# Kernel optimization log

Hardware: AMD Instinct MI355X
Metric: run time of the kernel (lower is better)

The kernel has to match this reference:

```python
import jax, jax.numpy as jnp
import numpy as np

K_NN = 20
EPS = 1e-5

def _conv1(x, w):
    # 1x1 Conv1d: w [O,C], x [B,C,N] -> [B,O,N]
    return jnp.einsum('oc,bcn->bon', w, x)

def _bn_eval(x, g, b):
    # BatchNorm1d in eval mode with running_mean=0, running_var=1
    return x * (g / np.sqrt(1.0 + EPS))[None, :, None] + b[None, :, None]

def _gn(x, g, b, groups=32):
    B, C, N = x.shape
    xr = x.reshape(B, groups, C // groups, N)
    mu = xr.mean(axis=(2, 3), keepdims=True)
    var = xr.var(axis=(2, 3), keepdims=True)
    xn = ((xr - mu) * jax.lax.rsqrt(var + EPS)).reshape(B, C, N)
    return xn * g[None, :, None] + b[None, :, None]

def _lrelu(x):
    return jnp.where(x >= 0, x, 0.2 * x)

def _graph_cross_attention(x, y, k):
    # x:[B,C,N] query features, y:[B,C,M] key features
    xn = x / jnp.linalg.norm(x, axis=1, keepdims=True)
    yn = y / jnp.linalg.norm(y, axis=1, keepdims=True)
    simi = jnp.einsum('bcn,bcm->bnm', xn, yn)          # cosine similarity [B,N,M]
    s, idx = jax.lax.top_k(simi, k)                    # [B,N,k] values and indices
    yt = jnp.swapaxes(y, 1, 2)                         # [B,M,C]
    nn = jax.vmap(lambda yb, ib: yb[ib])(yt, idx)      # gather neighbors [B,N,k,C]
    xt = jnp.swapaxes(x, 1, 2)                         # [B,N,C]
    diff = nn - xt[:, :, None, :]                      # edge features
    w = jax.nn.softmax(s, axis=-1)                     # attention over k neighbors
    agg = jnp.einsum('bnk,bnkc->bnc', w, diff)         # weighted aggregation
    return jnp.swapaxes(jnp.concatenate([xt, agg], axis=-1), 1, 2)  # [B,2C,N]

def setup_inputs() -> dict:
    key = jax.random.key(0)
    ks = jax.random.split(key, 22)
    B, N = 8, 2048
    f = lambda k, s: jax.random.normal(k, s, dtype=jnp.float32)
    return {
        'x1': f(ks[0], (B, 64, N)),
        'x2': f(ks[1], (B, 64, N)),
        'x3': f(ks[2], (B, 128, N)),
        'y3': f(ks[3], (B, 128, N)),
        'w4': f(ks[4], (256, 256)) * 0.06,
        'bn4_g': 1.0 + 0.1 * f(ks[5], (256,)),
        'bn4_b': 0.1 * f(ks[6], (256,)),
        'w5': f(ks[7], (512, 512)) * 0.04,
        'gn5_g': 1.0 + 0.1 * f(ks[8], (512,)),
        'gn5_b': 0.1 * f(ks[9], (512,)),
        'wm1': f(ks[10], (512, 512)) * 0.04,
        'bm1': 0.02 * f(ks[11], (512,)),
        'gn6_g': 1.0 + 0.1 * f(ks[12], (512,)),
        'gn6_b': 0.1 * f(ks[13], (512,)),
        'wm2': f(ks[14], (256, 512)) * 0.04,
        'bm2': 0.02 * f(ks[15], (256,)),
        'gn7_g': 1.0 + 0.1 * f(ks[16], (256,)),
        'gn7_b': 0.1 * f(ks[17], (256,)),
        'wm3': f(ks[18], (128, 256)) * 0.06,
        'bm3': 0.02 * f(ks[19], (128,)),
        'gn8_g': 1.0 + 0.1 * f(ks[20], (128,)),
        'gn8_b': 0.1 * f(ks[21], (128,)),
    }

def reference(x1, x2, x3, y3, w4, bn4_g, bn4_b, w5, gn5_g, gn5_b, wm1, bm1, gn6_g, gn6_b, wm2, bm2, gn7_g, gn7_b, wm3, bm3, gn8_g, gn8_b):
    x = _graph_cross_attention(x3, y3, K_NN)                  # [B,256,N]
    x4 = _lrelu(_bn_eval(_conv1(x, w4), bn4_g, bn4_b))        # conv4 [B,256,N]
    x = jnp.concatenate([x1, x2, x3, x4], axis=1)             # [B,512,N]
    local_concat = _lrelu(_gn(_conv1(x, w5), gn5_g, gn5_b))   # conv5 [B,512,N]
    gmax = local_concat.max(axis=2)
    gavg = local_concat.mean(axis=2)
    global_vector = jnp.concatenate([gmax, gavg], axis=1)     # [B,1024]
    h = jax.nn.relu(_gn(_conv1(local_concat, wm1) + bm1[None, :, None], gn6_g, gn6_b))
    h = jax.nn.relu(_gn(_conv1(h, wm2) + bm2[None, :, None], gn7_g, gn7_b))
    emb = jax.nn.relu(_gn(_conv1(h, wm3) + bm3[None, :, None], gn8_g, gn8_b))
    return emb, global_vector[:, :, None]
```

## Files before the change

kernel.cpp:

```cpp
#include <hip/hip_runtime.h>
#include <math.h>

#define N2 2048
#define LRELU_S 0.2f
#define BN4_RS 0.9999950000374997f

typedef short bf16x8 __attribute__((ext_vector_type(8)));
typedef float f32x16 __attribute__((ext_vector_type(16)));

__device__ __forceinline__ unsigned short bhi(float v) { return (unsigned short)(__float_as_uint(v) >> 16); }
__device__ __forceinline__ float bhif(float v) { return __uint_as_float(__float_as_uint(v) & 0xFFFF0000u); }
__device__ __forceinline__ float bf2f(unsigned short u) { return __uint_as_float(((unsigned int)u) << 16); }

__device__ __forceinline__ void gl16(const void* g, void* l) {
    __builtin_amdgcn_global_load_lds((const __attribute__((address_space(1))) unsigned int*)g,
                                     (__attribute__((address_space(3))) unsigned int*)l, 16, 0, 0);
}

__device__ __forceinline__ f32x16 z16() {
    f32x16 v;
    #pragma unroll
    for (int i = 0; i < 16; ++i) v[i] = 0.f;
    return v;
}

#define MFMA32 __builtin_amdgcn_mfma_f32_32x32x16_bf16

template<int ASRC, int EPI, int PASSES>
__global__ __launch_bounds__(256) void mgemm(
    const unsigned short* __restrict__ a1H, const unsigned short* __restrict__ a1L, int CA,
    const unsigned short* __restrict__ a2H, const unsigned short* __restrict__ a2L,
    const unsigned short* __restrict__ a3H, const unsigned short* __restrict__ a3L,
    const unsigned short* __restrict__ a4H, const unsigned short* __restrict__ a4L,
    const unsigned short* __restrict__ bH,  const unsigned short* __restrict__ bL, long bBs,
    int Ktot, int OC, int bbase,
    float* __restrict__ outF, unsigned short* __restrict__ oH,
    const float* __restrict__ epg, const float* __restrict__ epb,
    float* __restrict__ cs1, float* __restrict__ cs2)
{
    __shared__ alignas(16) unsigned short lAh[4096], lBh[4096];
    __shared__ alignas(16) unsigned short lAl[PASSES == 3 ? 4096 : 16];
    __shared__ alignas(16) unsigned short lBl[PASSES == 3 ? 4096 : 16];
    const int t  = threadIdx.x;
    const int n0 = blockIdx.x * 128;
    const int o0 = blockIdx.y * 128;
    const int bz = blockIdx.z;
    const int b  = bbase + bz;

    const int lane = t & 63;
    const int h    = lane >> 5;
    const int l31  = lane & 31;
    const int wid  = t >> 6;
    const int wm   = wid >> 1;
    const int wn   = wid & 1;
    const int sw   = (l31 >> 1) & 3;

    f32x16 acc00 = z16(), acc01 = z16(), acc10 = z16(), acc11 = z16();

    const int q0 = t, q1 = t + 256;
    const int r0 = q0 >> 2, p0 = q0 & 3, c0s = p0 ^ ((r0 >> 1) & 3);
    const int r1 = q1 >> 2, p1 = q1 & 3, c1s = p1 ^ ((r1 >> 1) & 3);

    const int rA0 = (wm * 64 + l31) * 32, rA1 = rA0 + 1024;
    const int rB0 = (wn * 64 + l31) * 32, rB1 = rB0 + 1024;

    for (int kc = 0; kc < Ktot; kc += 32) {
        const unsigned short *sAH, *sAL; int koff, Cs;
        if (ASRC == 0)      { sAH = a1H; sAL = a1L; koff = kc;       Cs = CA; }
        else if (ASRC == 1) {
            if (kc < 128)   { sAH = a1H; sAL = a1L; koff = kc;       Cs = 128; }
            else            { sAH = a2H; sAL = a2L; koff = kc - 128; Cs = 128; }
        } else {
            if (kc < 64)        { sAH = a1H; sAL = a1L; koff = kc;       Cs = 64;  }
            else if (kc < 128)  { sAH = a2H; sAL = a2L; koff = kc - 64;  Cs = 64;  }
            else if (kc < 256)  { sAH = a3H; sAL = a3L; koff = kc - 128; Cs = 128; }
            else                { sAH = a4H; sAL = a4L; koff = kc - 256; Cs = 256; }
        }
        __syncthreads();
        {
            long ga = ((long)b * N2 + n0 + r0) * Cs + koff + c0s * 8;
            long gb = (long)b * bBs + (long)(o0 + r0) * Ktot + kc + c0s * 8;
            gl16(sAH + ga, lAh + q0 * 8);
            gl16(bH + gb, lBh + q0 * 8);
            if (PASSES == 3) { gl16(sAL + ga, lAl + q0 * 8); gl16(bL + gb, lBl + q0 * 8); }
            long ga1 = ((long)b * N2 + n0 + r1) * Cs + koff + c1s * 8;
            long gb1 = (long)b * bBs + (long)(o0 + r1) * Ktot + kc + c1s * 8;
            gl16(sAH + ga1, lAh + q1 * 8);
            gl16(bH + gb1, lBh + q1 * 8);
            if (PASSES == 3) { gl16(sAL + ga1, lAl + q1 * 8); gl16(bL + gb1, lBl + q1 * 8); }
        }
        __syncthreads();
        #pragma unroll
        for (int s = 0; s < 2; ++s) {
            const int off = ((s * 2 + h) ^ sw) * 8;
            bf16x8 a0h = *(const bf16x8*)(lAh + rA0 + off);
            bf16x8 a1h_ = *(const bf16x8*)(lAh + rA1 + off);
            bf16x8 b0h = *(const bf16x8*)(lBh + rB0 + off);
            bf16x8 b1h = *(const bf16x8*)(lBh + rB1 + off);
            acc00 = MFMA32(a0h, b0h, acc00, 0, 0, 0);
            acc01 = MFMA32(a0h, b1h, acc01, 0, 0, 0);
            acc10 = MFMA32(a1h_, b0h, acc10, 0, 0, 0);
            acc11 = MFMA32(a1h_, b1h, acc11, 0, 0, 0);
            if (PASSES == 3) {
                bf16x8 a0l = *(const bf16x8*)(lAl + rA0 + off);
                bf16x8 a1l_ = *(const bf16x8*)(lAl + rA1 + off);
                bf16x8 b0l = *(const bf16x8*)(lBl + rB0 + off);
                bf16x8 b1l = *(const bf16x8*)(lBl + rB1 + off);
                acc00 = MFMA32(a0h, b0l, acc00, 0, 0, 0);
                acc00 = MFMA32(a0l, b0h, acc00, 0, 0, 0);
                acc01 = MFMA32(a0h, b1l, acc01, 0, 0, 0);
                acc01 = MFMA32(a0l, b1h, acc01, 0, 0, 0);
                acc10 = MFMA32(a1h_, b0l, acc10, 0, 0, 0);
                acc10 = MFMA32(a1l_, b0h, acc10, 0, 0, 0);
                acc11 = MFMA32(a1h_, b1l, acc11, 0, 0, 0);
                acc11 = MFMA32(a1l_, b1h, acc11, 0, 0, 0);
            }
        }
    }

    #pragma unroll
    for (int ni = 0; ni < 2; ++ni) {
        const int o = o0 + wn * 64 + ni * 32 + l31;
        float sc = 0.f, sh = 0.f, bias = 0.f;
        if (EPI == 1) { sc = epg[o] * BN4_RS; sh = epb[o]; }
        if (EPI == 2) { bias = epb ? epb[o] : 0.f; }
        float s1 = 0.f, s2 = 0.f;
        #pragma unroll
        for (int mi = 0; mi < 2; ++mi) {
            #pragma unroll
            for (int r = 0; r < 16; ++r) {
                const int n = n0 + wm * 64 + mi * 32 + (r & 3) + 8 * (r >> 2) + 4 * h;
                float v = (ni == 0) ? (mi == 0 ? acc00[r] : acc10[r])
                                    : (mi == 0 ? acc01[r] : acc11[r]);
                const long oi = ((long)bz * N2 + n) * (long)OC + o;
                if (EPI == 0) {
                    outF[oi] = v;
                } else if (EPI == 1) {
                    v = fmaf(v, sc, sh);
                    v = v >= 0.f ? v : LRELU_S * v;
                    oH[oi] = bhi(v);
                } else {
                    v += bias;
                    outF[oi] = v;
                    s1 += v; s2 = fmaf(v, v, s2);
                }
            }
        }
        if (EPI == 2) {
            s1 += __shfl_xor(s1, 32);
            s2 += __shfl_xor(s2, 32);
            if (h == 0) {
                atomicAdd(cs1 + bz * OC + o, s1);
                atomicAdd(cs2 + bz * OC + o, s2);
            }
        }
    }
}

__global__ void normK(const float* __restrict__ x3, const float* __restrict__ y3,
                      float* __restrict__ invnx, float* __restrict__ invny)
{
    const int n = blockIdx.x * 256 + threadIdx.x;
    const int b = blockIdx.y;
    const float* src = blockIdx.z ? y3 : x3;
    float ss = 0.f;
    for (int c = 0; c < 128; ++c) {
        float v = src[((long)b * 128 + c) * N2 + n];
        ss = fmaf(v, v, ss);
    }
    (blockIdx.z ? invny : invnx)[b * N2 + n] = rsqrtf(ss);
}

template<int MODE>
__global__ __launch_bounds__(256) void tsplitK(
    const float* __restrict__ in, int C,
    unsigned short* __restrict__ tHi, const float* __restrict__ invn,
    unsigned short* __restrict__ sHi, unsigned short* __restrict__ sLo,
    float* __restrict__ tF)
{
    __shared__ float lt[64 * 65];
    const int t = threadIdx.x;
    const int n0 = blockIdx.x * 64, c0 = blockIdx.y * 64, b = blockIdx.z;
    {
        const int nl = t & 63;
        const int cb = t >> 6;
        #pragma unroll
        for (int i = 0; i < 16; ++i) {
            const int cl = cb + 4 * i;
            lt[nl * 65 + cl] = in[((long)b * C + c0 + cl) * N2 + n0 + nl];
        }
    }
    __syncthreads();
    const int cl = t & 63;
    const int nb = t >> 6;
    #pragma unroll
    for (int i = 0; i < 16; ++i) {
        const int nl = nb + 4 * i;
        const float v = lt[nl * 65 + cl];
        const long oi = ((long)b * N2 + n0 + nl) * C + c0 + cl;
        if (MODE & 1) tHi[oi] = bhi(v);
        if (MODE & 2) {
            const float svv = v * invn[b * N2 + n0 + nl];
            sHi[oi] = bhi(svv); sLo[oi] = bhi(svv - bhif(svv));
        }
        if (MODE & 4) tF[oi] = v;
    }
}

__global__ void wsplitK(const float* __restrict__ w4, const float* __restrict__ w5,
    const float* __restrict__ wm1, const float* __restrict__ wm2, const float* __restrict__ wm3,
    unsigned short* __restrict__ w4h, unsigned short* __restrict__ w5h,
    unsigned short* __restrict__ m1h, unsigned short* __restrict__ m2h,
    unsigned short* __restrict__ m3h)
{
    const int y = blockIdx.y;
    const int idx = blockIdx.x * 256 + threadIdx.x;
    float v; unsigned short* dh;
    if (y == 0) {
        if (idx >= 256 * 256) return;
        const int k = idx & 255;
        v = w4[idx];
        if (k < 128) v -= w4[idx + 128];
        dh = w4h;
    } else if (y == 1) {
        if (idx >= 512 * 512) return;
        v = w5[idx]; dh = w5h;
    } else if (y == 2) {
        if (idx >= 512 * 512) return;
        v = wm1[idx]; dh = m1h;
    } else if (y == 3) {
        if (idx >= 256 * 512) return;
        v = wm2[idx]; dh = m2h;
    } else {
        if (idx >= 128 * 256) return;
        v = wm3[idx]; dh = m3h;
    }
    dh[idx] = bhi(v);
}

__global__ __launch_bounds__(256) void topkK(const float* __restrict__ simi,
    float* __restrict__ topw, int* __restrict__ topi, int bbase)
{
    __shared__ unsigned int hist[256];
    __shared__ unsigned int bcast[2];
    __shared__ float lmn[4], lmx[4];
    __shared__ unsigned int cnt0, candCnt, tick;
    __shared__ unsigned int candU[256];
    __shared__ float candV[256];
    __shared__ int   candI[256];
    __shared__ float selv[20];
    __shared__ int   seli[20];
    const int t  = threadIdx.x;
    const int n  = blockIdx.x;
    const int bl = blockIdx.y;
    const float* row = simi + ((long)bl * N2 + n) * N2;

    float    f[8];
    unsigned u[8];
    {
        const float4 v0 = *(const float4*)(row + 4 * t);
        const float4 v1 = *(const float4*)(row + 1024 + 4 * t);
        f[0] = v0.x; f[1] = v0.y; f[2] = v0.z; f[3] = v0.w;
        f[4] = v1.x; f[5] = v1.y; f[6] = v1.z; f[7] = v1.w;
        #pragma unroll
        for (int i = 0; i < 8; ++i) {
            unsigned ub = __float_as_uint(f[i]);
            u[i] = ub ^ (((int)ub >> 31) | 0x80000000u);
        }
    }

    float tmn = f[0], tmx = f[0];
    #pragma unroll
    for (int i = 1; i < 8; ++i) { tmn = fminf(tmn, f[i]); tmx = fmaxf(tmx, f[i]); }
    #pragma unroll
    for (int off = 1; off < 64; off <<= 1) {
        tmn = fminf(tmn, __shfl_xor(tmn, off));
        tmx = fmaxf(tmx, __shfl_xor(tmx, off));
    }
    if ((t & 63) == 0) { lmn[t >> 6] = tmn; lmx[t >> 6] = tmx; }
    if (t == 0) { cnt0 = 0; candCnt = 0; tick = 0; }
    hist[t] = 0;
    __syncthreads();
    const float rmn = fminf(fminf(lmn[0], lmn[1]), fminf(lmn[2], lmn[3]));
    const float rmx = fmaxf(fmaxf(lmx[0], lmx[1]), fmaxf(lmx[2], lmx[3]));
    const float rng = rmx - rmn;
    const float scale = (rng > 0.f) ? (255.0f / rng) : 0.f;

    int q[8];
    #pragma unroll
    for (int i = 0; i < 8; ++i) {
        int qi = (int)((f[i] - rmn) * scale);
        q[i] = qi < 0 ? 0 : (qi > 255 ? 255 : qi);
        atomicAdd(&hist[q[i]], 1u);
    }
    __syncthreads();

    if (t < 64) {
        const unsigned h0 = hist[4 * t], h1 = hist[4 * t + 1];
        const unsigned h2 = hist[4 * t + 2], h3 = hist[4 * t + 3];
        const unsigned s3 = h3, s2 = h2 + s3, s1 = h1 + s2, s0 = h0 + s1;
        unsigned inc = s0;
        #pragma unroll
        for (int off = 1; off < 64; off <<= 1) {
            const unsigned o = __shfl_down(inc, off);
            if (t + off < 64) inc += o;
        }
        const unsigned excl = inc - s0;
        const unsigned sf[5] = {excl + s0, excl + s1, excl + s2, excl + s3, excl};
        #pragma unroll
        for (int j = 0; j < 4; ++j) {
            if (sf[j] >= 20u && sf[j + 1] < 20u) {
                bcast[0] = 4 * t + j;
                bcast[1] = 20u - sf[j + 1];
            }
        }
    }
    __syncthreads();
    const int Abin   = (int)bcast[0];
    const int kneedA = (int)bcast[1];
    const int gt     = 20 - kneedA;

    #pragma unroll
    for (int i = 0; i < 8; ++i) {
        const int idx = (i < 4) ? (4 * t + i) : (1024 + 4 * t + (i - 4));
        if (q[i] > Abin) {
            const unsigned s = atomicAdd(&cnt0, 1u);
            selv[s] = f[i]; seli[s] = idx;
        } else if (q[i] == Abin) {
            const unsigned s = atomicAdd(&candCnt, 1u);
            if (s < 256u) { candU[s] = u[i]; candV[s] = f[i]; candI[s] = idx; }
        }
    }
    __syncthreads();

    const int cc = (int)candCnt;
    if (cc <= 256) {
        for (int slot = t; slot < cc; slot += 256) {
            const unsigned ui = candU[slot];
            int r = 0;
            for (int j = 0; j < cc; ++j) {
                const unsigned uj = candU[j];
                r += (uj > ui) || (uj == ui && j < slot);
            }
            if (r < kneedA) { selv[gt + r] = candV[slot]; seli[gt + r] = candI[slot]; }
        }
    } else {
        #pragma unroll
        for (int i = 0; i < 8; ++i) {
            const int idx = (i < 4) ? (4 * t + i) : (1024 + 4 * t + (i - 4));
            if (q[i] == Abin) {
                const unsigned e = atomicAdd(&tick, 1u);
                if ((int)e < kneedA) { selv[gt + e] = f[i]; seli[gt + e] = idx; }
            }
        }
    }
    __syncthreads();

    if (t < 64) {
        const float v = (t < 20) ? selv[t] : -1e30f;
        float m = v;
        #pragma unroll
        for (int off = 1; off < 32; off <<= 1) m = fmaxf(m, __shfl_xor(m, off, 32));
        const float e = (t < 20) ? expf(v - m) : 0.f;
        float s = e;
        #pragma unroll
        for (int off = 1; off < 32; off <<= 1) s += __shfl_xor(s, off, 32);
        if (t < 20) {
            const long base = (((long)(bbase + bl)) * N2 + n) * 20;
            topw[base + t] = e / s;
            topi[base + t] = seli[t];
        }
    }
}

__global__ __launch_bounds__(256) void aggK(const float* __restrict__ yT,
    const float* __restrict__ topw, const int* __restrict__ topi,
    unsigned short* __restrict__ Gh)
{
    const int t  = threadIdx.x;
    const int c4 = (t & 31) * 4;
    const int ns = t >> 5;
    const int b  = blockIdx.x;
    const int n  = blockIdx.y * 8 + ns;
    const long tb = ((long)b * N2 + n) * 20;
    const float* yb = yT + (long)b * N2 * 128 + c4;

    float a0 = 0.f, a1 = 0.f, a2 = 0.f, a3 = 0.f;
    #pragma unroll
    for (int k = 0; k < 20; ++k) {
        const float w  = topw[tb + k];
        const int  idx = topi[tb + k];
        const float4 v = *(const float4*)(yb + (long)idx * 128);
        a0 = fmaf(w, v.x, a0);
        a1 = fmaf(w, v.y, a1);
        a2 = fmaf(w, v.z, a2);
        a3 = fmaf(w, v.w, a3);
    }
    const long oi = ((long)b * N2 + n) * 128 + c4;
    ushort4 hh;
    hh.x = bhi(a0); hh.y = bhi(a1); hh.z = bhi(a2); hh.w = bhi(a3);
    *(ushort4*)(Gh + oi) = hh;
}

__global__ void statsK(const float* __restrict__ cs1, const float* __restrict__ cs2,
    float* __restrict__ stats, int C)
{
    const int t = threadIdx.x;
    const int b = t >> 5, g = t & 31;
    const int cpg = C >> 5;
    float s1 = 0.f, s2 = 0.f;
    for (int j = 0; j < cpg; ++j) {
        s1 += cs1[b * C + g * cpg + j];
        s2 += cs2[b * C + g * cpg + j];
    }
    const float cnt = (float)(cpg * N2);
    const float mu = s1 / cnt;
    const float var = s2 / cnt - mu * mu;
    stats[t * 2] = mu;
    stats[t * 2 + 1] = rsqrtf(var + 1e-5f);
}

template<int ACT, int LC>
__global__ void gnapplyK(const float* __restrict__ pre, const float* __restrict__ stats,
    const float* __restrict__ gamma, const float* __restrict__ beta,
    unsigned short* __restrict__ oH)
{
    const long i4 = ((long)blockIdx.x * 256 + threadIdx.x) * 4;
    const int C = 1 << LC;
    const int c = (int)(i4 & (C - 1));
    const int bn = (int)(i4 >> LC);
    const int b = bn >> 11;
    const int g = c >> (LC - 5);
    const float mu = stats[(b * 32 + g) * 2];
    const float rs = stats[(b * 32 + g) * 2 + 1];
    const float4 gm = *(const float4*)(gamma + c);
    const float4 bt = *(const float4*)(beta + c);
    const float4 v = *(const float4*)(pre + i4);
    const float vals[4] = {v.x, v.y, v.z, v.w};
    const float gms[4] = {gm.x, gm.y, gm.z, gm.w};
    const float bts[4] = {bt.x, bt.y, bt.z, bt.w};
    unsigned short hs[4];
    #pragma unroll
    for (int j = 0; j < 4; ++j) {
        float x = (vals[j] - mu) * (rs * gms[j]) + bts[j];
        x = (ACT == 0) ? (x >= 0.f ? x : LRELU_S * x) : (x >= 0.f ? x : 0.f);
        hs[j] = bhi(x);
    }
    ushort4 hh; hh.x = hs[0]; hh.y = hs[1]; hh.z = hs[2]; hh.w = hs[3];
    *(ushort4*)(oH + i4) = hh;
}

__global__ __launch_bounds__(256) void gnfinalK(const float* __restrict__ pre,
    const float* __restrict__ stats, const float* __restrict__ gamma,
    const float* __restrict__ beta, float* __restrict__ out)
{
    __shared__ float lt[64 * 65];
    const int t = threadIdx.x;
    const int n0 = blockIdx.x * 64, c0 = blockIdx.y * 64, b = blockIdx.z;
    {
        const int cl = t & 63;
        const int nb = t >> 6;
        const int c = c0 + cl;
        const int g = c >> 2;
        const float mu = stats[(b * 32 + g) * 2];
        const float rs = stats[(b * 32 + g) * 2 + 1];
        const float sc = rs * gamma[c], sh = beta[c] - mu * sc;
        #pragma unroll
        for (int i = 0; i < 16; ++i) {
            const int nl = nb + 4 * i;
            float v = pre[((long)b * N2 + n0 + nl) * 128 + c];
            v = v * sc + sh;
            lt[cl * 65 + nl] = v > 0.f ? v : 0.f;
        }
    }
    __syncthreads();
    const int nl = t & 63;
    const int cb = t >> 6;
    #pragma unroll
    for (int i = 0; i < 16; ++i) {
        const int cl = cb + 4 * i;
        out[((long)b * 128 + c0 + cl) * N2 + n0 + nl] = lt[cl * 65 + nl];
    }
}

__global__ __launch_bounds__(256) void pool1K(const unsigned short* __restrict__ lcH,
    float* __restrict__ pmax, float* __restrict__ psum)
{
    __shared__ float lmx[512], lsm[512];
    const int t  = threadIdx.x;
    const int cq = t & 127;
    const int rp = t >> 7;
    const int nch = blockIdx.x;
    const int b   = blockIdx.y;
    float mx[4] = {-1e30f, -1e30f, -1e30f, -1e30f};
    float sm[4] = {0.f, 0.f, 0.f, 0.f};
    for (int i = 0; i < 32; ++i) {
        const int n = nch * 64 + 2 * i + rp;
        const long base = ((long)b * N2 + n) * 512 + cq * 4;
        const ushort4 hh = *(const ushort4*)(lcH + base);
        const float v0 = bf2f(hh.x);
        const float v1 = bf2f(hh.y);
        const float v2 = bf2f(hh.z);
        const float v3 = bf2f(hh.w);
        mx[0] = fmaxf(mx[0], v0); sm[0] += v0;
        mx[1] = fmaxf(mx[1], v1); sm[1] += v1;
        mx[2] = fmaxf(mx[2], v2); sm[2] += v2;
        mx[3] = fmaxf(mx[3], v3); sm[3] += v3;
    }
    if (rp) {
        #pragma unroll
        for (int j = 0; j < 4; ++j) { lmx[cq * 4 + j] = mx[j]; lsm[cq * 4 + j] = sm[j]; }
    }
    __syncthreads();
    if (!rp) {
        const long pb = ((long)(b * 32 + nch)) * 512 + cq * 4;
        #pragma unroll
        for (int j = 0; j < 4; ++j) {
            pmax[pb + j] = fmaxf(mx[j], lmx[cq * 4 + j]);
            psum[pb + j] = sm[j] + lsm[cq * 4 + j];
        }
    }
}

__global__ void pool2K(const float* __restrict__ pmax, const float* __restrict__ psum,
                       float* __restrict__ gv)
{
    const int t = threadIdx.x;
    const int b = blockIdx.x;
    float mx0 = -1e30f, mx1 = -1e30f, s0 = 0.f, s1 = 0.f;
    for (int nch = 0; nch < 32; ++nch) {
        const long pb = ((long)(b * 32 + nch)) * 512 + 2 * t;
        const float2 pm = *(const float2*)(pmax + pb);
        const float2 ps = *(const float2*)(psum + pb);
        mx0 = fmaxf(mx0, pm.x); mx1 = fmaxf(mx1, pm.y);
        s0 += ps.x; s1 += ps.y;
    }
    gv[b * 1024 + 2 * t]           = mx0;
    gv[b * 1024 + 2 * t + 1]       = mx1;
    gv[b * 1024 + 512 + 2 * t]     = s0 * (1.f / 2048.f);
    gv[b * 1024 + 512 + 2 * t + 1] = s1 * (1.f / 2048.f);
}

extern "C" void kernel_launch(void* const* d_in, const int* in_sizes, int n_in,
                              void* d_out, int out_size, void* d_ws, size_t ws_size,
                              hipStream_t stream)
{
    const float* x1    = (const float*)d_in[0];
    const float* x2    = (const float*)d_in[1];
    const float* x3    = (const float*)d_in[2];
    const float* y3    = (const float*)d_in[3];
    const float* w4    = (const float*)d_in[4];
    const float* bn4g  = (const float*)d_in[5];
    const float* bn4b  = (const float*)d_in[6];
    const float* w5    = (const float*)d_in[7];
    const float* gn5g  = (const float*)d_in[8];
    const float* gn5b  = (const float*)d_in[9];
    const float* wm1   = (const float*)d_in[10];
    const float* bm1   = (const float*)d_in[11];
    const float* gn6g  = (const float*)d_in[12];
    const float* gn6b  = (const float*)d_in[13];
    const float* wm2   = (const float*)d_in[14];
    const float* bm2   = (const float*)d_in[15];
    const float* gn7g  = (const float*)d_in[16];
    const float* gn7b  = (const float*)d_in[17];
    const float* wm3   = (const float*)d_in[18];
    const float* bm3   = (const float*)d_in[19];
    const float* gn8g  = (const float*)d_in[20];
    const float* gn8b  = (const float*)d_in[21];
    float* out = (float*)d_out;
    (void)in_sizes; (void)n_in; (void)out_size; (void)ws_size;

    char* ws = (char*)d_ws;
    float*          simiF = (float*)(ws + 0);
    float*          bufPS = (float*)(ws + 0);
    unsigned short* lcH   = (unsigned short*)(ws + 134217728);
    unsigned short* h1H   = (unsigned short*)(ws + 150994944);
    unsigned short* x4H   = (unsigned short*)(ws + 167772160);
    unsigned short* h2H   = (unsigned short*)(ws + 176160768);
    float*          yT    = (float*)(ws + 184549376);
    unsigned short* x3tH  = (unsigned short*)(ws + 192937984);
    unsigned short* GH    = (unsigned short*)(ws + 197132288);
    unsigned short* xnH   = (unsigned short*)(ws + 201326592);
    unsigned short* xnL   = (unsigned short*)(ws + 205520896);
    unsigned short* ynH   = (unsigned short*)(ws + 209715200);
    unsigned short* ynL   = (unsigned short*)(ws + 213909504);
    unsigned short* x1tH  = (unsigned short*)(ws + 218103808);
    unsigned short* x2tH  = (unsigned short*)(ws + 220200960);
    unsigned short* w4pH  = (unsigned short*)(ws + 222298112);
    unsigned short* w5H   = (unsigned short*)(ws + 222429184);
    unsigned short* m1H   = (unsigned short*)(ws + 222953472);
    unsigned short* m2H   = (unsigned short*)(ws + 223477760);
    unsigned short* m3H   = (unsigned short*)(ws + 223739904);
    float* invnx = (float*)(ws + 223805440);
    float* invny = (float*)(ws + 223870976);
    float* topw  = (float*)(ws + 223936512);
    int*   topi  = (int*)  (ws + 225247232);
    float* csb   = (float*)(ws + 226557952);
    float* cs1_5 = csb,          *cs2_5 = csb + 4096;
    float* cs1_6 = csb + 8192,   *cs2_6 = csb + 12288;
    float* cs1_7 = csb + 16384,  *cs2_7 = csb + 20480;
    float* cs1_8 = csb + 24576,  *cs2_8 = csb + 28672;
    float* stats5 = (float*)(ws + 226689024);
    float* stats6 = stats5 + 512;
    float* stats7 = stats5 + 1024;
    float* stats8 = stats5 + 1536;
    float* pmax  = (float*)(ws + 226697216);
    float* psum  = (float*)(ws + 227221504);

    const dim3 B256(256);
    const unsigned short* nu = nullptr;

    hipMemsetAsync(csb, 0, 131072, stream);

    normK<<<dim3(8, 8, 2), B256, 0, stream>>>(x3, y3, invnx, invny);
    tsplitK<6><<<dim3(32, 2, 8), B256, 0, stream>>>(y3, 128, nullptr, invny, ynH, ynL, yT);
    tsplitK<3><<<dim3(32, 2, 8), B256, 0, stream>>>(x3, 128, x3tH, invnx, xnH, xnL, nullptr);
    tsplitK<1><<<dim3(32, 1, 8), B256, 0, stream>>>(x1, 64, x1tH, nullptr, nullptr, nullptr, nullptr);
    tsplitK<1><<<dim3(32, 1, 8), B256, 0, stream>>>(x2, 64, x2tH, nullptr, nullptr, nullptr, nullptr);
    wsplitK<<<dim3(1024, 5), B256, 0, stream>>>(w4, w5, wm1, wm2, wm3,
        w4pH, w5H, m1H, m2H, m3H);

    mgemm<0, 0, 3><<<dim3(16, 16, 8), B256, 0, stream>>>(
        xnH, xnL, 128, nu, nu, nu, nu, nu, nu,
        ynH, ynL, (long)N2 * 128, 128, 2048, 0,
        simiF, nullptr, nullptr, nullptr, nullptr, nullptr);
    topkK<<<dim3(2048, 8), B256, 0, stream>>>(simiF, topw, topi, 0);

    aggK<<<dim3(8, 256), B256, 0, stream>>>(yT, topw, topi, GH);

    mgemm<1, 1, 1><<<dim3(16, 2, 8), B256, 0, stream>>>(
        x3tH, nu, 128, GH, nu, nu, nu, nu, nu,
        w4pH, nu, 0, 256, 256, 0,
        nullptr, x4H, bn4g, bn4b, nullptr, nullptr);

    mgemm<2, 2, 1><<<dim3(16, 4, 8), B256, 0, stream>>>(
        x1tH, nu, 64, x2tH, nu, x3tH, nu, x4H, nu,
        w5H, nu, 0, 512, 512, 0,
        bufPS, nullptr, nullptr, nullptr, cs1_5, cs2_5);
    statsK<<<1, B256, 0, stream>>>(cs1_5, cs2_5, stats5, 512);
    gnapplyK<0, 9><<<8192, B256, 0, stream>>>(bufPS, stats5, gn5g, gn5b, lcH);

    pool1K<<<dim3(32, 8), B256, 0, stream>>>(lcH, pmax, psum);
    pool2K<<<dim3(8), B256, 0, stream>>>(pmax, psum, out + (long)8 * 128 * 2048);

    mgemm<0, 2, 1><<<dim3(16, 4, 8), B256, 0, stream>>>(
        lcH, nu, 512, nu, nu, nu, nu, nu, nu,
        m1H, nu, 0, 512, 512, 0,
        bufPS, nullptr, nullptr, bm1, cs1_6, cs2_6);
    statsK<<<1, B256, 0, stream>>>(cs1_6, cs2_6, stats6, 512);
    gnapplyK<1, 9><<<8192, B256, 0, stream>>>(bufPS, stats6, gn6g, gn6b, h1H);

    mgemm<0, 2, 1><<<dim3(16, 2, 8), B256, 0, stream>>>(
        h1H, nu, 512, nu, nu, nu, nu, nu, nu,
        m2H, nu, 0, 512, 256, 0,
        bufPS, nullptr, nullptr, bm2, cs1_7, cs2_7);
    statsK<<<1, B256, 0, stream>>>(cs1_7, cs2_7, stats7, 256);
    gnapplyK<1, 8><<<4096, B256, 0, stream>>>(bufPS, stats7, gn7g, gn7b, h2H);

    mgemm<0, 2, 1><<<dim3(16, 1, 8), B256, 0, stream>>>(
        h2H, nu, 256, nu, nu, nu, nu, nu, nu,
        m3H, nu, 0, 256, 128, 0,
        bufPS, nullptr, nullptr, bm3, cs1_8, cs2_8);
    statsK<<<1, B256, 0, stream>>>(cs1_8, cs2_8, stats8, 128);
    gnfinalK<<<dim3(32, 2, 8), B256, 0, stream>>>(bufPS, stats8, gn8g, gn8b, out);
}
```

Measured before the change: 358.2 us.

## Fuse norm into transpose, fold GN stats into apply, add nontemporal simi traffic

The separate row-norm kernel is merged into a single transpose kernel that stages all 128 channels in LDS, computes the inverse norm there, and writes the normalized hi/lo bf16 splits. The two 64-channel transposes are merged into one launch. The four single-block statsK launches are removed; each GroupNorm apply block now recomputes its group mean and rstd from the channel sums. Nontemporal store and load hints are added on the similarity matrix write and its read in top-k. Together this cuts about six kernel launches and one pass over x3/y3, at the cost of redundant per-block stats work and a larger LDS tile in the transpose.

Measured after the change: 325.8 us. 1.1x faster.

```diff
diff --git a/kernel.cpp b/kernel.cpp
--- a/kernel.cpp
+++ b/kernel.cpp
@@ -7,6 +7,7 @@
 
 typedef short bf16x8 __attribute__((ext_vector_type(8)));
 typedef float f32x16 __attribute__((ext_vector_type(16)));
+typedef float f32x4 __attribute__((ext_vector_type(4)));
 
 __device__ __forceinline__ unsigned short bhi(float v) { return (unsigned short)(__float_as_uint(v) >> 16); }
 __device__ __forceinline__ float bhif(float v) { return __uint_as_float(__float_as_uint(v) & 0xFFFF0000u); }
@@ -134,7 +135,7 @@
                                     : (mi == 0 ? acc01[r] : acc11[r]);
                 const long oi = ((long)bz * N2 + n) * (long)OC + o;
                 if (EPI == 0) {
-                    outF[oi] = v;
+                    __builtin_nontemporal_store(v, outF + oi);
                 } else if (EPI == 1) {
                     v = fmaf(v, sc, sh);
                     v = v >= 0.f ? v : LRELU_S * v;
@@ -157,37 +158,67 @@
     }
 }
 
-__global__ void normK(const float* __restrict__ x3, const float* __restrict__ y3,
-                      float* __restrict__ invnx, float* __restrict__ invny)
-{
-    const int n = blockIdx.x * 256 + threadIdx.x;
-    const int b = blockIdx.y;
-    const float* src = blockIdx.z ? y3 : x3;
-    float ss = 0.f;
-    for (int c = 0; c < 128; ++c) {
-        float v = src[((long)b * 128 + c) * N2 + n];
-        ss = fmaf(v, v, ss);
-    }
-    (blockIdx.z ? invny : invnx)[b * N2 + n] = rsqrtf(ss);
-}
-
 template<int MODE>
-__global__ __launch_bounds__(256) void tsplitK(
-    const float* __restrict__ in, int C,
-    unsigned short* __restrict__ tHi, const float* __restrict__ invn,
-    unsigned short* __restrict__ sHi, unsigned short* __restrict__ sLo,
-    float* __restrict__ tF)
-{
-    __shared__ float lt[64 * 65];
+__global__ __launch_bounds__(256) void tnormK(
+    const float* __restrict__ in,
+    unsigned short* __restrict__ tHi, float* __restrict__ tF,
+    unsigned short* __restrict__ sHi, unsigned short* __restrict__ sLo)
+{
+    __shared__ float lt[64 * 130];
+    __shared__ float pinv[64];
     const int t = threadIdx.x;
-    const int n0 = blockIdx.x * 64, c0 = blockIdx.y * 64, b = blockIdx.z;
+    const int n0 = blockIdx.x * 64, b = blockIdx.z;
     {
         const int nl = t & 63;
         const int cb = t >> 6;
         #pragma unroll
+        for (int i = 0; i < 32; ++i) {
+            const int cl = cb + 4 * i;
+            lt[nl * 130 + cl] = in[((long)b * 128 + cl) * N2 + n0 + nl];
+        }
+    }
+    __syncthreads();
+    if (t < 64) {
+        float ss = 0.f;
+        for (int c = 0; c < 128; ++c) {
+            const float v = lt[t * 130 + c];
+            ss = fmaf(v, v, ss);
+        }
+        pinv[t] = rsqrtf(ss);
+    }
+    __syncthreads();
+    const int cl = t & 127;
+    const int nb = t >> 7;
+    #pragma unroll
+    for (int i = 0; i < 32; ++i) {
+        const int nl = nb + 2 * i;
+        const float v = lt[nl * 130 + cl];
+        const float sv = v * pinv[nl];
+        const long oi = ((long)b * N2 + n0 + nl) * 128 + cl;
+        sHi[oi] = bhi(sv); sLo[oi] = bhi(sv - bhif(sv));
+        if (MODE & 1) tHi[oi] = bhi(v);
+        if (MODE & 4) tF[oi] = v;
+    }
+}
+
+__global__ __launch_bounds__(256) void t64K(
+    const float* __restrict__ x1, const float* __restrict__ x2,
+    unsigned short* __restrict__ o1, unsigned short* __restrict__ o2)
+{
+    __shared__ float lt[64 * 65];
+    const int t = threadIdx.x;
+    const int z = blockIdx.z;
+    const int b = z & 7;
+    const float* in = (z < 8) ? x1 : x2;
+    unsigned short* outp = (z < 8) ? o1 : o2;
+    const int n0 = blockIdx.x * 64;
+    {
+        const int nl = t & 63;
+        const int cb = t >> 6;
+        #pragma unroll
         for (int i = 0; i < 16; ++i) {
             const int cl = cb + 4 * i;
-            lt[nl * 65 + cl] = in[((long)b * C + c0 + cl) * N2 + n0 + nl];
+            lt[nl * 65 + cl] = in[((long)b * 64 + cl) * N2 + n0 + nl];
         }
     }
     __syncthreads();
@@ -196,14 +227,7 @@
     #pragma unroll
     for (int i = 0; i < 16; ++i) {
         const int nl = nb + 4 * i;
-        const float v = lt[nl * 65 + cl];
-        const long oi = ((long)b * N2 + n0 + nl) * C + c0 + cl;
-        if (MODE & 1) tHi[oi] = bhi(v);
-        if (MODE & 2) {
-            const float svv = v * invn[b * N2 + n0 + nl];
-            sHi[oi] = bhi(svv); sLo[oi] = bhi(svv - bhif(svv));
-        }
-        if (MODE & 4) tF[oi] = v;
+        outp[((long)b * N2 + n0 + nl) * 64 + cl] = bhi(lt[nl * 65 + cl]);
     }
 }
 
@@ -258,10 +282,10 @@
     float    f[8];
     unsigned u[8];
     {
-        const float4 v0 = *(const float4*)(row + 4 * t);
-        const float4 v1 = *(const float4*)(row + 1024 + 4 * t);
-        f[0] = v0.x; f[1] = v0.y; f[2] = v0.z; f[3] = v0.w;
-        f[4] = v1.x; f[5] = v1.y; f[6] = v1.z; f[7] = v1.w;
+        const f32x4 v0 = __builtin_nontemporal_load((const f32x4*)(row + 4 * t));
+        const f32x4 v1 = __builtin_nontemporal_load((const f32x4*)(row + 1024 + 4 * t));
+        f[0] = v0[0]; f[1] = v0[1]; f[2] = v0[2]; f[3] = v0[3];
+        f[4] = v1[0]; f[5] = v1[1]; f[6] = v1[2]; f[7] = v1[3];
         #pragma unroll
         for (int i = 0; i < 8; ++i) {
             unsigned ub = __float_as_uint(f[i]);
@@ -402,37 +426,35 @@
     *(ushort4*)(Gh + oi) = hh;
 }
 
-__global__ void statsK(const float* __restrict__ cs1, const float* __restrict__ cs2,
-    float* __restrict__ stats, int C)
-{
-    const int t = threadIdx.x;
-    const int b = t >> 5, g = t & 31;
-    const int cpg = C >> 5;
-    float s1 = 0.f, s2 = 0.f;
-    for (int j = 0; j < cpg; ++j) {
-        s1 += cs1[b * C + g * cpg + j];
-        s2 += cs2[b * C + g * cpg + j];
-    }
-    const float cnt = (float)(cpg * N2);
-    const float mu = s1 / cnt;
-    const float var = s2 / cnt - mu * mu;
-    stats[t * 2] = mu;
-    stats[t * 2 + 1] = rsqrtf(var + 1e-5f);
-}
-
 template<int ACT, int LC>
-__global__ void gnapplyK(const float* __restrict__ pre, const float* __restrict__ stats,
+__global__ void gnapplyK(const float* __restrict__ pre,
+    const float* __restrict__ cs1, const float* __restrict__ cs2,
     const float* __restrict__ gamma, const float* __restrict__ beta,
     unsigned short* __restrict__ oH)
 {
-    const long i4 = ((long)blockIdx.x * 256 + threadIdx.x) * 4;
+    __shared__ float smu[32], srs[32];
     const int C = 1 << LC;
+    const int cpg = C >> 5;
+    const long blockBase = (long)blockIdx.x * 1024;
+    const int b = (int)(blockBase >> (LC + 11));
+    const int t = threadIdx.x;
+    if (t < 32) {
+        float s1 = 0.f, s2 = 0.f;
+        for (int j = 0; j < cpg; ++j) {
+            s1 += cs1[b * C + t * cpg + j];
+            s2 += cs2[b * C + t * cpg + j];
+        }
+        const float cnt = (float)(cpg * N2);
+        const float mu = s1 / cnt;
+        const float var = s2 / cnt - mu * mu;
+        smu[t] = mu; srs[t] = rsqrtf(var + 1e-5f);
+    }
+    __syncthreads();
+    const long i4 = blockBase + t * 4;
     const int c = (int)(i4 & (C - 1));
-    const int bn = (int)(i4 >> LC);
-    const int b = bn >> 11;
     const int g = c >> (LC - 5);
-    const float mu = stats[(b * 32 + g) * 2];
-    const float rs = stats[(b * 32 + g) * 2 + 1];
+    const float mu = smu[g];
+    const float rs = srs[g];
     const float4 gm = *(const float4*)(gamma + c);
     const float4 bt = *(const float4*)(beta + c);
     const float4 v = *(const float4*)(pre + i4);
@@ -451,19 +473,33 @@
 }
 
 __global__ __launch_bounds__(256) void gnfinalK(const float* __restrict__ pre,
-    const float* __restrict__ stats, const float* __restrict__ gamma,
-    const float* __restrict__ beta, float* __restrict__ out)
+    const float* __restrict__ cs1, const float* __restrict__ cs2,
+    const float* __restrict__ gamma, const float* __restrict__ beta,
+    float* __restrict__ out)
 {
     __shared__ float lt[64 * 65];
+    __shared__ float smu[16], srs[16];
     const int t = threadIdx.x;
     const int n0 = blockIdx.x * 64, c0 = blockIdx.y * 64, b = blockIdx.z;
+    if (t < 16) {
+        const int g = (c0 >> 2) + t;
+        float s1 = 0.f, s2 = 0.f;
+        for (int j = 0; j < 4; ++j) {
+            s1 += cs1[b * 128 + g * 4 + j];
+            s2 += cs2[b * 128 + g * 4 + j];
+        }
+        const float cnt = (float)(4 * N2);
+        const float mu = s1 / cnt;
+        const float var = s2 / cnt - mu * mu;
+        smu[t] = mu; srs[t] = rsqrtf(var + 1e-5f);
+    }
+    __syncthreads();
     {
         const int cl = t & 63;
         const int nb = t >> 6;
         const int c = c0 + cl;
-        const int g = c >> 2;
-        const float mu = stats[(b * 32 + g) * 2];
-        const float rs = stats[(b * 32 + g) * 2 + 1];
+        const float mu = smu[cl >> 2];
+        const float rs = srs[cl >> 2];
         const float sc = rs * gamma[c], sh = beta[c] - mu * sc;
         #pragma unroll
         for (int i = 0; i < 16; ++i) {
@@ -591,8 +627,6 @@
     unsigned short* m1H   = (unsigned short*)(ws + 222953472);
     unsigned short* m2H   = (unsigned short*)(ws + 223477760);
     unsigned short* m3H   = (unsigned short*)(ws + 223739904);
-    float* invnx = (float*)(ws + 223805440);
-    float* invny = (float*)(ws + 223870976);
     float* topw  = (float*)(ws + 223936512);
     int*   topi  = (int*)  (ws + 225247232);
     float* csb   = (float*)(ws + 226557952);
@@ -600,10 +634,6 @@
     float* cs1_6 = csb + 8192,   *cs2_6 = csb + 12288;
     float* cs1_7 = csb + 16384,  *cs2_7 = csb + 20480;
     float* cs1_8 = csb + 24576,  *cs2_8 = csb + 28672;
-    float* stats5 = (float*)(ws + 226689024);
-    float* stats6 = stats5 + 512;
-    float* stats7 = stats5 + 1024;
-    float* stats8 = stats5 + 1536;
     float* pmax  = (float*)(ws + 226697216);
     float* psum  = (float*)(ws + 227221504);
 
@@ -612,11 +642,9 @@
 
     hipMemsetAsync(csb, 0, 131072, stream);
 
-    normK<<<dim3(8, 8, 2), B256, 0, stream>>>(x3, y3, invnx, invny);
-    tsplitK<6><<<dim3(32, 2, 8), B256, 0, stream>>>(y3, 128, nullptr, invny, ynH, ynL, yT);
-    tsplitK<3><<<dim3(32, 2, 8), B256, 0, stream>>>(x3, 128, x3tH, invnx, xnH, xnL, nullptr);
-    tsplitK<1><<<dim3(32, 1, 8), B256, 0, stream>>>(x1, 64, x1tH, nullptr, nullptr, nullptr, nullptr);
-    tsplitK<1><<<dim3(32, 1, 8), B256, 0, stream>>>(x2, 64, x2tH, nullptr, nullptr, nullptr, nullptr);
+    tnormK<4><<<dim3(32, 1, 8), B256, 0, stream>>>(y3, nullptr, yT, ynH, ynL);
+    tnormK<1><<<dim3(32, 1, 8), B256, 0, stream>>>(x3, x3tH, nullptr, xnH, xnL);
+    t64K<<<dim3(32, 1, 16), B256, 0, stream>>>(x1, x2, x1tH, x2tH);
     wsplitK<<<dim3(1024, 5), B256, 0, stream>>>(w4, w5, wm1, wm2, wm3,
         w4pH, w5H, m1H, m2H, m3H);
 
@@ -637,8 +665,7 @@
         x1tH, nu, 64, x2tH, nu, x3tH, nu, x4H, nu,
         w5H, nu, 0, 512, 512, 0,
         bufPS, nullptr, nullptr, nullptr, cs1_5, cs2_5);
-    statsK<<<1, B256, 0, stream>>>(cs1_5, cs2_5, stats5, 512);
-    gnapplyK<0, 9><<<8192, B256, 0, stream>>>(bufPS, stats5, gn5g, gn5b, lcH);
+    gnapplyK<0, 9><<<8192, B256, 0, stream>>>(bufPS, cs1_5, cs2_5, gn5g, gn5b, lcH);
 
     pool1K<<<dim3(32, 8), B256, 0, stream>>>(lcH, pmax, psum);
     pool2K<<<dim3(8), B256, 0, stream>>>(pmax, psum, out + (long)8 * 128 * 2048);
@@ -647,20 +674,17 @@
         lcH, nu, 512, nu, nu, nu, nu, nu, nu,
         m1H, nu, 0, 512, 512, 0,
         bufPS, nullptr, nullptr, bm1, cs1_6, cs2_6);
-    statsK<<<1, B256, 0, stream>>>(cs1_6, cs2_6, stats6, 512);
-    gnapplyK<1, 9><<<8192, B256, 0, stream>>>(bufPS, stats6, gn6g, gn6b, h1H);
+    gnapplyK<1, 9><<<8192, B256, 0, stream>>>(bufPS, cs1_6, cs2_6, gn6g, gn6b, h1H);
 
     mgemm<0, 2, 1><<<dim3(16, 2, 8), B256, 0, stream>>>(
         h1H, nu, 512, nu, nu, nu, nu, nu, nu,
         m2H, nu, 0, 512, 256, 0,
         bufPS, nullptr, nullptr, bm2, cs1_7, cs2_7);
-    statsK<<<1, B256, 0, stream>>>(cs1_7, cs2_7, stats7, 256);
-    gnapplyK<1, 8><<<4096, B256, 0, stream>>>(bufPS, stats7, gn7g, gn7b, h2H);
+    gnapplyK<1, 8><<<4096, B256, 0, stream>>>(bufPS, cs1_7, cs2_7, gn7g, gn7b, h2H);
 
     mgemm<0, 2, 1><<<dim3(16, 1, 8), B256, 0, stream>>>(
         h2H, nu, 256, nu, nu, nu, nu, nu, nu,
         m3H, nu, 0, 256, 128, 0,
         bufPS, nullptr, nullptr, bm3, cs1_8, cs2_8);
-    statsK<<<1, B256, 0, stream>>>(cs1_8, cs2_8, stats8, 128);
-    gnfinalK<<<dim3(32, 2, 8), B256, 0, stream>>>(bufPS, stats8, gn8g, gn8b, out);
-}
+    gnfinalK<<<dim3(32, 2, 8), B256, 0, stream>>>(bufPS, cs1_8, cs2_8, gn8g, gn8b, out);
+}
```
